# Kernel tuning notes

Measured on AMD Instinct MI355X. Metric: run time of the kernel, lower is better.

Reference implementation:

```python
import jax, jax.numpy as jnp
import numpy as np

T, B = 21, 4096
H, E, V = 1024, 50, 96
PAD = 0


def setup_inputs() -> dict:
    key = jax.random.key(0)
    ks = jax.random.split(key, 10)
    s_e = 1.0 / np.sqrt(H)  # torch LSTM init scale
    emb = jax.random.normal(ks[0], (V, E), jnp.float32)
    emb = emb.at[PAD].set(0.0)  # padding_idx row is zero
    return {
        "input_ids": jax.random.randint(ks[1], (T, B), 0, V),
        "h0": jax.random.normal(ks[2], (1, B, H), jnp.float32),
        "c0": jax.random.normal(ks[3], (1, B, H), jnp.float32),
        "emb": emb,
        "W_ih": jax.random.uniform(ks[4], (4 * H, E), jnp.float32, -s_e, s_e),
        "W_hh": jax.random.uniform(ks[5], (4 * H, H), jnp.float32, -s_e, s_e),
        "b_ih": jax.random.uniform(ks[6], (4 * H,), jnp.float32, -s_e, s_e),
        "b_hh": jax.random.uniform(ks[7], (4 * H,), jnp.float32, -s_e, s_e),
        "W_out": jax.random.uniform(ks[8], (V, H), jnp.float32, -s_e, s_e),
        "b_out": jax.random.uniform(ks[9], (V,), jnp.float32, -s_e, s_e),
    }


def reference(input_ids, h0, c0, emb, W_ih, W_hh, b_ih, b_hh, W_out, b_out):
    # char_embeds: (T, B, E)
    x = emb[input_ids]
    # Precompute input projections for all timesteps in one GEMM: (T, B, 4H)
    x_proj = jnp.einsum("tbe,ge->tbg", x, W_ih) + b_ih + b_hh

    def step(carry, xp_t):
        h, c = carry  # (B, H) each
        gates = xp_t + h @ W_hh.T  # (B, 4H), torch gate order i,f,g,o
        i, f, g, o = jnp.split(gates, 4, axis=-1)
        i = jax.nn.sigmoid(i)
        f = jax.nn.sigmoid(f)
        g = jnp.tanh(g)
        o = jax.nn.sigmoid(o)
        c = f * c + i * g
        h = o * jnp.tanh(c)
        return (h, c), h

    (h_T, c_T), h_ts = jax.lax.scan(step, (h0[0], c0[0]), x_proj)
    # char_output_projection: (T, B, V)
    scores = jnp.einsum("tbh,vh->tbv", h_ts, W_out) + b_out
    return scores, (h_T[None], c_T[None])
```

## Files before the change

kernel.cpp:

```cpp
#include <hip/hip_runtime.h>
#include <hip/hip_bf16.h>


#define T_STEPS 21
#define BSZ 4096
#define HDIM 1024
#define VOCAB 96
#define EDIM 50

typedef __attribute__((ext_vector_type(8))) short short8;
typedef __attribute__((ext_vector_type(4))) short shortx4;
typedef __attribute__((ext_vector_type(4))) float f32x4;

#define GLL16(g, l)                                                        \
  __builtin_amdgcn_global_load_lds(                                        \
      (const __attribute__((address_space(1))) void*)(g),                  \
      (__attribute__((address_space(3))) void*)(l), 16, 0, 0)

#define ASM_BARRIER() asm volatile("s_barrier" ::: "memory")
#define ASM_VMCNT4() asm volatile("s_waitcnt vmcnt(4)" ::: "memory")
#define ASM_VMCNT0() asm volatile("s_waitcnt vmcnt(0)" ::: "memory")

__device__ __forceinline__ float sigmoidf_fast(float x) {
  return 1.0f / (1.0f + __expf(-x));
}
__device__ __forceinline__ float tanhf_fast(float x) {
  return 2.0f / (1.0f + __expf(-2.0f * x)) - 1.0f;
}
__device__ __forceinline__ float b2f(short s) {
  return __uint_as_float(((unsigned int)(unsigned short)s) << 16);
}

__global__ void prep_convert(const float* __restrict__ Whh_f,
                             const float* __restrict__ Wout_f,
                             const float* __restrict__ h0,
                             __hip_bfloat16* __restrict__ Whh,
                             __hip_bfloat16* __restrict__ Wout,
                             __hip_bfloat16* __restrict__ hb0) {
  int idx = blockIdx.x * 256 + threadIdx.x;
  if (idx < 4 * HDIM * HDIM) {
    Whh[idx] = __float2bfloat16(Whh_f[idx]);
    hb0[idx] = __float2bfloat16(h0[idx]);
  }
  if (idx < VOCAB * HDIM) Wout[idx] = __float2bfloat16(Wout_f[idx]);
}

__global__ void prep_ptable(const float* __restrict__ emb,
                            const float* __restrict__ Wih,
                            const float* __restrict__ bih,
                            const float* __restrict__ bhh,
                            __hip_bfloat16* __restrict__ Pb) {
  int idx = blockIdx.x * 256 + threadIdx.x;
  int v = idx >> 12, g = idx & 4095;
  int gate = g >> 10, j = g & 1023;
  const float* er = emb + v * EDIM;
  const float* wr = Wih + g * EDIM;
  float s = bih[g] + bhh[g];
#pragma unroll 10
  for (int e = 0; e < EDIM; ++e) s += er[e] * wr[e];
  Pb[(size_t)(j >> 6) * 24576 + v * 256 + (j & 63) * 4 + gate] =
      __float2bfloat16(s);
}


#define STAGE_A(h, kt, b)                                                   \
  do {                                                                      \
    GLL16(hprev + aSrc[0] + (size_t)(h) * 131072 + (size_t)(kt) * 64,       \
          smem + ((b) << 16) + ((h) << 14) + aDst[0]);                      \
    GLL16(hprev + aSrc[1] + (size_t)(h) * 131072 + (size_t)(kt) * 64,       \
          smem + ((b) << 16) + ((h) << 14) + aDst[1]);                      \
  } while (0)

#define STAGE_B(h, kt, b)                                                   \
  do {                                                                      \
    GLL16(Whh + bSrc[h][0] + (size_t)(kt) * 64,                             \
          smem + ((b) << 16) + bDst[h][0]);                                 \
    GLL16(Whh + bSrc[h][1] + (size_t)(kt) * 64,                             \
          smem + ((b) << 16) + bDst[h][1]);                                 \
  } while (0)

#define PHASE(mh, nh, STAGE_STMT, VM_STMT)                                  \
  {                                                                         \
    short8 af[8], bf[4];                                                    \
    _Pragma("unroll") for (int mi2 = 0; mi2 < 4; ++mi2) {                   \
      af[mi2] = *(const short8*)&cA[((mh) * 128 + wr * 64 + mi2 * 16 +      \
                                     u16) * 64 + sl0];                      \
      af[4 + mi2] = *(const short8*)&cA[((mh) * 128 + wr * 64 + mi2 * 16 +  \
                                         u16) * 64 + sl1];                  \
    }                                                                       \
    _Pragma("unroll") for (int ni2 = 0; ni2 < 2; ++ni2) {                   \
      bf[ni2] = *(const short8*)&cB[(wc * 64 + (nh) * 32 + ni2 * 16 +       \
                                     u16) * 64 + sl0];                      \
      bf[2 + ni2] = *(const short8*)&cB[(wc * 64 + (nh) * 32 + ni2 * 16 +   \
                                         u16) * 64 + sl1];                  \
    }                                                                       \
    STAGE_STMT;                                                             \
    ASM_BARRIER();                                                          \
    __builtin_amdgcn_s_setprio(1);                                          \
    _Pragma("unroll") for (int mi2 = 0; mi2 < 4; ++mi2)                     \
        _Pragma("unroll") for (int ni2 = 0; ni2 < 2; ++ni2) {               \
      acc[(mh) * 4 + mi2][(nh) * 2 + ni2] =                                 \
          __builtin_amdgcn_mfma_f32_16x16x32_bf16(                          \
              af[mi2], bf[ni2], acc[(mh) * 4 + mi2][(nh) * 2 + ni2],        \
              0, 0, 0);                                                     \
      acc[(mh) * 4 + mi2][(nh) * 2 + ni2] =                                 \
          __builtin_amdgcn_mfma_f32_16x16x32_bf16(                          \
              af[4 + mi2], bf[2 + ni2],                                     \
              acc[(mh) * 4 + mi2][(nh) * 2 + ni2], 0, 0, 0);                \
    }                                                                       \
    __builtin_amdgcn_s_setprio(0);                                          \
    VM_STMT;                                                                \
    ASM_BARRIER();                                                          \
  }

template <bool LAST>
__global__ __launch_bounds__(512, 2) void lstm_step_kernel(
    const int* __restrict__ ids,
    const __hip_bfloat16* __restrict__ hprev,
    const __hip_bfloat16* __restrict__ Whh,
    const __hip_bfloat16* __restrict__ Pb,
    const float* __restrict__ c_in,
    float* __restrict__ c_out,
    __hip_bfloat16* __restrict__ hnext,
    float* __restrict__ hf32)
{
  __shared__ __align__(16) char smem[131072];

  const int tid = threadIdx.x;
  const int wid = tid >> 6;
  const int lane = tid & 63;
  const int wr = wid >> 2;
  const int wc = wid & 3;
  const int u16 = lane & 15;
  const int k16q = lane >> 4;
  const int u7 = u16 & 7;
  const int sl0 = (k16q ^ u7) * 8;
  const int sl1 = ((4 + k16q) ^ u7) * 8;

  const int bid = blockIdx.x;
  const int mt = (bid & 7) * 2 + ((bid >> 3) & 1);
  const int jt = bid >> 4;
  const int m0 = mt * 256;

  const int lrow = lane >> 3;
  const int swcol = ((lane & 7) ^ lrow) * 8;

  size_t aSrc[2];
  size_t bSrc[2][2];
  int aDst[2];
  int bDst[2][2];
#pragma unroll
  for (int q = 0; q < 2; ++q) {
    const int g = wid * 2 + q;
    aSrc[q] = (size_t)(m0 + g * 8 + lrow) * HDIM + swcol;
    aDst[q] = g * 1024;
#pragma unroll
    for (int h = 0; h < 2; ++h) {
      const int R = (g >> 2) * 64 + h * 32 + (g & 3) * 8;
      const int n = R + lrow;
      const int gate = (n >> 4) & 3;
      const int uo = (n >> 6) * 16 + (n & 15);
      bSrc[h][q] = (size_t)(gate * HDIM + jt * 64 + uo) * HDIM + swcol;
      bDst[h][q] = 32768 + R * 128;
    }
  }

  STAGE_A(0, 0, 0);
  STAGE_B(0, 0, 0);
  STAGE_A(1, 0, 0);
  STAGE_B(1, 0, 0);
  STAGE_A(0, 1, 1);
  STAGE_B(0, 1, 1);

  ASM_VMCNT4();
  ASM_BARRIER();

  f32x4 acc[8][4] = {};

#pragma unroll 2
  for (int k = 0; k < 16; ++k) {
    const int b = k & 1;
    const int nb = b ^ 1;
    const __hip_bfloat16* cA = (const __hip_bfloat16*)(smem + (b << 16));
    const __hip_bfloat16* cB =
        (const __hip_bfloat16*)(smem + (b << 16) + 32768);

    PHASE(0, 0, { if (k < 15) STAGE_A(1, k + 1, nb); }, {});
    PHASE(0, 1, { if (k < 15) STAGE_B(1, k + 1, nb); }, {});
    PHASE(1, 0, { if (k < 14) STAGE_A(0, k + 2, b); }, {});
    PHASE(1, 1, { if (k < 14) STAGE_B(0, k + 2, b); }, {
      if (k < 14) {
        ASM_VMCNT4();
      } else if (k == 14) {
        ASM_VMCNT0();
      }
    });
  }

  const int jcol = jt * 64 + wc * 16 + u16;
  float cpre[8][4];
#pragma unroll
  for (int mi = 0; mi < 8; ++mi)
#pragma unroll
    for (int r = 0; r < 4; ++r)
      cpre[mi][r] = c_in[(size_t)(m0 + (mi >> 2) * 128 + wr * 64 +
                                  (mi & 3) * 16 + k16q * 4 + r) *
                             HDIM +
                         jcol];

  {
    const __hip_bfloat16* Pbj = Pb + (size_t)jt * 24576;
#pragma unroll
    for (int i = 0; i < 6; ++i)
      GLL16(Pbj + (wid * 6 + i) * 512 + lane * 8,
            smem + (wid * 6 + i) * 1024);
  }
  ASM_VMCNT0();
  ASM_BARRIER();

  const __hip_bfloat16* sPb = (const __hip_bfloat16*)smem;
  const int uo4 = (wc * 16 + u16) * 4;
  const int rb = m0 + wr * 64 + k16q * 4;
#pragma unroll
  for (int mi = 0; mi < 8; ++mi) {
#pragma unroll
    for (int r = 0; r < 4; ++r) {
      const int row = rb + (mi >> 2) * 128 + (mi & 3) * 16 + r;
      const int id = ids[row];
      const shortx4 pv = *(const shortx4*)&sPb[id * 256 + uo4];
      float iv = acc[mi][0][r] + b2f(pv[0]);
      float fv = acc[mi][1][r] + b2f(pv[1]);
      float gv = acc[mi][2][r] + b2f(pv[2]);
      float ov = acc[mi][3][r] + b2f(pv[3]);
      iv = sigmoidf_fast(iv);
      fv = sigmoidf_fast(fv);
      gv = tanhf_fast(gv);
      ov = sigmoidf_fast(ov);
      const size_t off = (size_t)row * HDIM + jcol;
      const float cc = fv * cpre[mi][r] + iv * gv;
      c_out[off] = cc;
      const float hh = ov * tanhf_fast(cc);
      hnext[off] = __float2bfloat16(hh);
      if (LAST) hf32[off] = hh;
    }
  }
}

__global__ __launch_bounds__(256, 2) void scores_kernel(
    const __hip_bfloat16* __restrict__ h,
    const __hip_bfloat16* __restrict__ Wout,
    const float* __restrict__ bout,
    float* __restrict__ out)
{
  __shared__ __align__(16) __hip_bfloat16 sA[128 * 128];
  __shared__ __align__(16) __hip_bfloat16 sB[96 * 128];

  const int tid = threadIdx.x;
  const int wave = tid >> 6, lane = tid & 63;
  const int u16 = lane & 15, k16q = lane >> 4;
  const long r0 = (long)blockIdx.x * 128;

  f32x4 acc[2][6] = {};

  const int srow4 = lane >> 4;
  const int sslot = lane & 15;

  for (int k0 = 0; k0 < HDIM; k0 += 128) {
#pragma unroll
    for (int i = 0; i < 8; ++i) {
      int row = wave * 32 + i * 4 + srow4;
      int gg = sslot ^ (row & 15);
      GLL16(h + (r0 + row) * HDIM + k0 + gg * 8,
            &sA[(wave * 32 + i * 4) * 128]);
    }
#pragma unroll
    for (int i = 0; i < 6; ++i) {
      int row = wave * 24 + i * 4 + srow4;
      int gg = sslot ^ (row & 15);
      GLL16(Wout + (size_t)row * HDIM + k0 + gg * 8,
            &sB[(wave * 24 + i * 4) * 128]);
    }
    __syncthreads();
#pragma unroll
    for (int kk = 0; kk < 128; kk += 32) {
      const int sl = (((kk >> 3) + k16q) ^ u16) * 8;
      short8 af[2], bf[6];
#pragma unroll
      for (int mi = 0; mi < 2; ++mi)
        af[mi] = *(const short8*)&sA[(wave * 32 + mi * 16 + u16) * 128 + sl];
#pragma unroll
      for (int ni = 0; ni < 6; ++ni)
        bf[ni] = *(const short8*)&sB[(ni * 16 + u16) * 128 + sl];
#pragma unroll
      for (int mi = 0; mi < 2; ++mi)
#pragma unroll
        for (int ni = 0; ni < 6; ++ni)
          acc[mi][ni] = __builtin_amdgcn_mfma_f32_16x16x32_bf16(
              af[mi], bf[ni], acc[mi][ni], 0, 0, 0);
    }
    __syncthreads();
  }

#pragma unroll
  for (int ni = 0; ni < 6; ++ni) {
    int v = ni * 16 + u16;
    float bv = bout[v];
#pragma unroll
    for (int mi = 0; mi < 2; ++mi)
#pragma unroll
      for (int r = 0; r < 4; ++r) {
        long grow = r0 + wave * 32 + mi * 16 + k16q * 4 + r;
        out[grow * VOCAB + v] = acc[mi][ni][r] + bv;
      }
  }
}

extern "C" void kernel_launch(void* const* d_in, const int* in_sizes, int n_in,
                              void* d_out, int out_size, void* d_ws,
                              size_t ws_size, hipStream_t stream) {
  const int* ids = (const int*)d_in[0];
  const float* h0 = (const float*)d_in[1];
  const float* c0 = (const float*)d_in[2];
  const float* emb = (const float*)d_in[3];
  const float* Wih = (const float*)d_in[4];
  const float* Whh_f = (const float*)d_in[5];
  const float* bih = (const float*)d_in[6];
  const float* bhh = (const float*)d_in[7];
  const float* Wout_f = (const float*)d_in[8];
  const float* bout = (const float*)d_in[9];

  float* out = (float*)d_out;
  float* scores = out;
  float* hT = out + (size_t)T_STEPS * BSZ * VOCAB;
  float* cT = hT + (size_t)BSZ * HDIM;

  const size_t BH = (size_t)BSZ * HDIM;
  char* w = (char*)d_ws;
  __hip_bfloat16* Pb = (__hip_bfloat16*)w;   w += (size_t)16 * 24576 * 2;
  __hip_bfloat16* Whh = (__hip_bfloat16*)w;  w += (size_t)4 * HDIM * HDIM * 2;
  __hip_bfloat16* Wout = (__hip_bfloat16*)w; w += (size_t)VOCAB * HDIM * 2;
  __hip_bfloat16* hts = (__hip_bfloat16*)w;
  size_t base = (size_t)16 * 24576 * 2 + (size_t)4 * HDIM * HDIM * 2 +
                (size_t)VOCAB * HDIM * 2;
  const bool full = ws_size >= base + (size_t)(T_STEPS + 1) * BH * 2;

  prep_convert<<<dim3((4 * HDIM * HDIM + 255) / 256), dim3(256), 0, stream>>>(
      Whh_f, Wout_f, h0, Whh, Wout, hts);
  prep_ptable<<<dim3((VOCAB * 4096) / 256), dim3(256), 0, stream>>>(
      emb, Wih, bih, bhh, Pb);

  for (int t = 0; t < T_STEPS; ++t) {
    __hip_bfloat16* hp = hts + (full ? (size_t)t * BH : (size_t)(t & 1) * BH);
    __hip_bfloat16* hn =
        hts + (full ? (size_t)(t + 1) * BH : (size_t)((t + 1) & 1) * BH);
    const float* cin = (t == 0) ? c0 : cT;
    if (t == T_STEPS - 1) {
      lstm_step_kernel<true><<<dim3(256), dim3(512), 0, stream>>>(
          ids + (size_t)t * BSZ, hp, Whh, Pb, cin, cT, hn, hT);
    } else {
      lstm_step_kernel<false><<<dim3(256), dim3(512), 0, stream>>>(
          ids + (size_t)t * BSZ, hp, Whh, Pb, cin, cT, hn, nullptr);
    }
    if (!full) {
      scores_kernel<<<dim3(BSZ / 128), dim3(256), 0, stream>>>(
          hn, Wout, bout, scores + (size_t)t * BSZ * VOCAB);
    }
  }
  if (full) {
    scores_kernel<<<dim3(T_STEPS * BSZ / 128), dim3(256), 0, stream>>>(
        hts + BH, Wout, bout, scores);
  }
}
```

Baseline: 1.162 ms.

## Fuse LSTM timesteps into one persistent kernel with per-row-tile grid barriers

Replaces the 21 per-timestep LSTM kernel launches with a single persistent kernel of 256 blocks that loops over time. Each block synchronises only with the 16 blocks sharing its batch row tile through an atomic counter barrier. This removes launch overhead and the full-device drain between steps. It relies on all 256 blocks being co-resident (2 per CU via launch bounds) to avoid deadlock, and on counters reset in the prep kernel.

Measured after the change: 1.991 ms. 1.71x slower.

```diff
diff --git a/kernel.cpp b/kernel.cpp
--- a/kernel.cpp
+++ b/kernel.cpp
@@ -36,8 +36,10 @@
                              const float* __restrict__ h0,
                              __hip_bfloat16* __restrict__ Whh,
                              __hip_bfloat16* __restrict__ Wout,
-                             __hip_bfloat16* __restrict__ hb0) {
+                             __hip_bfloat16* __restrict__ hb0,
+                             int* __restrict__ bars) {
   int idx = blockIdx.x * 256 + threadIdx.x;
+  if (blockIdx.x == 0 && threadIdx.x < 16) bars[threadIdx.x] = 0;
   if (idx < 4 * HDIM * HDIM) {
     Whh[idx] = __float2bfloat16(Whh_f[idx]);
     hb0[idx] = __float2bfloat16(h0[idx]);
@@ -62,7 +64,6 @@
       __float2bfloat16(s);
 }
 
-
 #define STAGE_A(h, kt, b)                                                   \
   do {                                                                      \
     GLL16(hprev + aSrc[0] + (size_t)(h) * 131072 + (size_t)(kt) * 64,       \
@@ -113,137 +114,163 @@
     ASM_BARRIER();                                                          \
   }
 
+#define LSTM_SETUP()                                                        \
+  const int tid = threadIdx.x;                                              \
+  const int wid = tid >> 6;                                                 \
+  const int lane = tid & 63;                                                \
+  const int wr = wid >> 2;                                                  \
+  const int wc = wid & 3;                                                   \
+  const int u16 = lane & 15;                                                \
+  const int k16q = lane >> 4;                                               \
+  const int u7 = u16 & 7;                                                   \
+  const int sl0 = (k16q ^ u7) * 8;                                          \
+  const int sl1 = ((4 + k16q) ^ u7) * 8;                                    \
+  const int bid = blockIdx.x;                                               \
+  const int mt = (bid & 7) * 2 + ((bid >> 3) & 1);                          \
+  const int jt = bid >> 4;                                                  \
+  const int m0 = mt * 256;                                                  \
+  const int lrow = lane >> 3;                                               \
+  const int swcol = ((lane & 7) ^ lrow) * 8;                                \
+  size_t aSrc[2];                                                           \
+  size_t bSrc[2][2];                                                        \
+  int aDst[2];                                                              \
+  int bDst[2][2];                                                           \
+  _Pragma("unroll") for (int q = 0; q < 2; ++q) {                           \
+    const int g = wid * 2 + q;                                              \
+    aSrc[q] = (size_t)(m0 + g * 8 + lrow) * HDIM + swcol;                   \
+    aDst[q] = g * 1024;                                                     \
+    _Pragma("unroll") for (int h = 0; h < 2; ++h) {                         \
+      const int R = (g >> 2) * 64 + h * 32 + (g & 3) * 8;                   \
+      const int n = R + lrow;                                               \
+      const int gate = (n >> 4) & 3;                                        \
+      const int uo = (n >> 6) * 16 + (n & 15);                              \
+      bSrc[h][q] = (size_t)(gate * HDIM + jt * 64 + uo) * HDIM + swcol;     \
+      bDst[h][q] = 32768 + R * 128;                                         \
+    }                                                                       \
+  }
+
+#define LSTM_STEP_BODY(IS_LAST)                                             \
+  {                                                                         \
+    STAGE_A(0, 0, 0);                                                       \
+    STAGE_B(0, 0, 0);                                                       \
+    STAGE_A(1, 0, 0);                                                       \
+    STAGE_B(1, 0, 0);                                                       \
+    STAGE_A(0, 1, 1);                                                       \
+    STAGE_B(0, 1, 1);                                                       \
+    ASM_VMCNT4();                                                           \
+    ASM_BARRIER();                                                          \
+    f32x4 acc[8][4] = {};                                                   \
+    _Pragma("unroll 2") for (int k = 0; k < 16; ++k) {                      \
+      const int b = k & 1;                                                  \
+      const int nb = b ^ 1;                                                 \
+      const __hip_bfloat16* cA = (const __hip_bfloat16*)(smem + (b << 16)); \
+      const __hip_bfloat16* cB =                                            \
+          (const __hip_bfloat16*)(smem + (b << 16) + 32768);                \
+      PHASE(0, 0, { if (k < 15) STAGE_A(1, k + 1, nb); }, {});              \
+      PHASE(0, 1, { if (k < 15) STAGE_B(1, k + 1, nb); }, {});              \
+      PHASE(1, 0, { if (k < 14) STAGE_A(0, k + 2, b); }, {});               \
+      PHASE(1, 1, { if (k < 14) STAGE_B(0, k + 2, b); }, {                  \
+        if (k < 14) { ASM_VMCNT4(); } else if (k == 14) { ASM_VMCNT0(); }   \
+      });                                                                   \
+    }                                                                       \
+    const int jcol = jt * 64 + wc * 16 + u16;                               \
+    float cpre[8][4];                                                       \
+    _Pragma("unroll") for (int mi = 0; mi < 8; ++mi)                        \
+        _Pragma("unroll") for (int r = 0; r < 4; ++r)                       \
+            cpre[mi][r] = c_in_p[(size_t)(m0 + (mi >> 2) * 128 + wr * 64 +  \
+                                          (mi & 3) * 16 + k16q * 4 + r) *   \
+                                     HDIM +                                 \
+                                 jcol];                                     \
+    {                                                                       \
+      const __hip_bfloat16* Pbj = Pb + (size_t)jt * 24576;                  \
+      _Pragma("unroll") for (int i = 0; i < 6; ++i)                         \
+          GLL16(Pbj + (wid * 6 + i) * 512 + lane * 8,                       \
+                smem + (wid * 6 + i) * 1024);                               \
+    }                                                                       \
+    ASM_VMCNT0();                                                           \
+    ASM_BARRIER();                                                          \
+    const __hip_bfloat16* sPb = (const __hip_bfloat16*)smem;                \
+    const int uo4 = (wc * 16 + u16) * 4;                                    \
+    const int rb = m0 + wr * 64 + k16q * 4;                                 \
+    _Pragma("unroll") for (int mi = 0; mi < 8; ++mi) {                      \
+      _Pragma("unroll") for (int r = 0; r < 4; ++r) {                       \
+        const int row = rb + (mi >> 2) * 128 + (mi & 3) * 16 + r;           \
+        const int id = ids_t[row];                                          \
+        const shortx4 pv = *(const shortx4*)&sPb[id * 256 + uo4];           \
+        float iv = acc[mi][0][r] + b2f(pv[0]);                              \
+        float fv = acc[mi][1][r] + b2f(pv[1]);                              \
+        float gv = acc[mi][2][r] + b2f(pv[2]);                              \
+        float ov = acc[mi][3][r] + b2f(pv[3]);                              \
+        iv = sigmoidf_fast(iv);                                             \
+        fv = sigmoidf_fast(fv);                                             \
+        gv = tanhf_fast(gv);                                                \
+        ov = sigmoidf_fast(ov);                                             \
+        const size_t off = (size_t)row * HDIM + jcol;                       \
+        const float cc = fv * cpre[mi][r] + iv * gv;                        \
+        c_out_p[off] = cc;                                                  \
+        const float hh = ov * tanhf_fast(cc);                               \
+        hnext[off] = __float2bfloat16(hh);                                  \
+        if (IS_LAST) hf32_p[off] = hh;                                      \
+      }                                                                     \
+    }                                                                       \
+  }
+
+__global__ __launch_bounds__(512, 2) void lstm_persistent(
+    const int* __restrict__ ids,
+    const __hip_bfloat16* __restrict__ Whh,
+    const __hip_bfloat16* __restrict__ Pb,
+    const float* __restrict__ c0,
+    float* __restrict__ cT,
+    __hip_bfloat16* __restrict__ hts,
+    float* __restrict__ hT,
+    int* __restrict__ bars)
+{
+  __shared__ __align__(16) char smem[131072];
+  LSTM_SETUP();
+  const size_t BH = (size_t)BSZ * HDIM;
+
+#pragma unroll 1
+  for (int t = 0; t < T_STEPS; ++t) {
+    const __hip_bfloat16* hprev = hts + (size_t)t * BH;
+    __hip_bfloat16* hnext = hts + (size_t)(t + 1) * BH;
+    const float* c_in_p = (t == 0) ? c0 : cT;
+    float* c_out_p = cT;
+    const int* ids_t = ids + (size_t)t * BSZ;
+    float* hf32_p = hT;
+    const bool last = (t == T_STEPS - 1);
+
+    LSTM_STEP_BODY(last);
+
+    if (t < T_STEPS - 1) {
+      __syncthreads();
+      if (tid == 0) {
+        __hip_atomic_fetch_add(&bars[mt], 1, __ATOMIC_RELEASE,
+                               __HIP_MEMORY_SCOPE_AGENT);
+        const int target = 16 * (t + 1);
+        while (__hip_atomic_fetch_add(&bars[mt], 0, __ATOMIC_RELAXED,
+                                      __HIP_MEMORY_SCOPE_AGENT) < target)
+          __builtin_amdgcn_s_sleep(2);
+        (void)__hip_atomic_load(&bars[mt], __ATOMIC_ACQUIRE,
+                                __HIP_MEMORY_SCOPE_AGENT);
+      }
+      __syncthreads();
+    }
+  }
+}
+
 template <bool LAST>
 __global__ __launch_bounds__(512, 2) void lstm_step_kernel(
-    const int* __restrict__ ids,
+    const int* __restrict__ ids_t,
     const __hip_bfloat16* __restrict__ hprev,
     const __hip_bfloat16* __restrict__ Whh,
     const __hip_bfloat16* __restrict__ Pb,
-    const float* __restrict__ c_in,
-    float* __restrict__ c_out,
+    const float* __restrict__ c_in_p,
+    float* __restrict__ c_out_p,
     __hip_bfloat16* __restrict__ hnext,
-    float* __restrict__ hf32)
-{
+    float* __restrict__ hf32_p) {
   __shared__ __align__(16) char smem[131072];
-
-  const int tid = threadIdx.x;
-  const int wid = tid >> 6;
-  const int lane = tid & 63;
-  const int wr = wid >> 2;
-  const int wc = wid & 3;
-  const int u16 = lane & 15;
-  const int k16q = lane >> 4;
-  const int u7 = u16 & 7;
-  const int sl0 = (k16q ^ u7) * 8;
-  const int sl1 = ((4 + k16q) ^ u7) * 8;
-
-  const int bid = blockIdx.x;
-  const int mt = (bid & 7) * 2 + ((bid >> 3) & 1);
-  const int jt = bid >> 4;
-  const int m0 = mt * 256;
-
-  const int lrow = lane >> 3;
-  const int swcol = ((lane & 7) ^ lrow) * 8;
-
-  size_t aSrc[2];
-  size_t bSrc[2][2];
-  int aDst[2];
-  int bDst[2][2];
-#pragma unroll
-  for (int q = 0; q < 2; ++q) {
-    const int g = wid * 2 + q;
-    aSrc[q] = (size_t)(m0 + g * 8 + lrow) * HDIM + swcol;
-    aDst[q] = g * 1024;
-#pragma unroll
-    for (int h = 0; h < 2; ++h) {
-      const int R = (g >> 2) * 64 + h * 32 + (g & 3) * 8;
-      const int n = R + lrow;
-      const int gate = (n >> 4) & 3;
-      const int uo = (n >> 6) * 16 + (n & 15);
-      bSrc[h][q] = (size_t)(gate * HDIM + jt * 64 + uo) * HDIM + swcol;
-      bDst[h][q] = 32768 + R * 128;
-    }
-  }
-
-  STAGE_A(0, 0, 0);
-  STAGE_B(0, 0, 0);
-  STAGE_A(1, 0, 0);
-  STAGE_B(1, 0, 0);
-  STAGE_A(0, 1, 1);
-  STAGE_B(0, 1, 1);
-
-  ASM_VMCNT4();
-  ASM_BARRIER();
-
-  f32x4 acc[8][4] = {};
-
-#pragma unroll 2
-  for (int k = 0; k < 16; ++k) {
-    const int b = k & 1;
-    const int nb = b ^ 1;
-    const __hip_bfloat16* cA = (const __hip_bfloat16*)(smem + (b << 16));
-    const __hip_bfloat16* cB =
-        (const __hip_bfloat16*)(smem + (b << 16) + 32768);
-
-    PHASE(0, 0, { if (k < 15) STAGE_A(1, k + 1, nb); }, {});
-    PHASE(0, 1, { if (k < 15) STAGE_B(1, k + 1, nb); }, {});
-    PHASE(1, 0, { if (k < 14) STAGE_A(0, k + 2, b); }, {});
-    PHASE(1, 1, { if (k < 14) STAGE_B(0, k + 2, b); }, {
-      if (k < 14) {
-        ASM_VMCNT4();
-      } else if (k == 14) {
-        ASM_VMCNT0();
-      }
-    });
-  }
-
-  const int jcol = jt * 64 + wc * 16 + u16;
-  float cpre[8][4];
-#pragma unroll
-  for (int mi = 0; mi < 8; ++mi)
-#pragma unroll
-    for (int r = 0; r < 4; ++r)
-      cpre[mi][r] = c_in[(size_t)(m0 + (mi >> 2) * 128 + wr * 64 +
-                                  (mi & 3) * 16 + k16q * 4 + r) *
-                             HDIM +
-                         jcol];
-
-  {
-    const __hip_bfloat16* Pbj = Pb + (size_t)jt * 24576;
-#pragma unroll
-    for (int i = 0; i < 6; ++i)
-      GLL16(Pbj + (wid * 6 + i) * 512 + lane * 8,
-            smem + (wid * 6 + i) * 1024);
-  }
-  ASM_VMCNT0();
-  ASM_BARRIER();
-
-  const __hip_bfloat16* sPb = (const __hip_bfloat16*)smem;
-  const int uo4 = (wc * 16 + u16) * 4;
-  const int rb = m0 + wr * 64 + k16q * 4;
-#pragma unroll
-  for (int mi = 0; mi < 8; ++mi) {
-#pragma unroll
-    for (int r = 0; r < 4; ++r) {
-      const int row = rb + (mi >> 2) * 128 + (mi & 3) * 16 + r;
-      const int id = ids[row];
-      const shortx4 pv = *(const shortx4*)&sPb[id * 256 + uo4];
-      float iv = acc[mi][0][r] + b2f(pv[0]);
-      float fv = acc[mi][1][r] + b2f(pv[1]);
-      float gv = acc[mi][2][r] + b2f(pv[2]);
-      float ov = acc[mi][3][r] + b2f(pv[3]);
-      iv = sigmoidf_fast(iv);
-      fv = sigmoidf_fast(fv);
-      gv = tanhf_fast(gv);
-      ov = sigmoidf_fast(ov);
-      const size_t off = (size_t)row * HDIM + jcol;
-      const float cc = fv * cpre[mi][r] + iv * gv;
-      c_out[off] = cc;
-      const float hh = ov * tanhf_fast(cc);
-      hnext[off] = __float2bfloat16(hh);
-      if (LAST) hf32[off] = hh;
-    }
-  }
+  LSTM_SETUP();
+  LSTM_STEP_BODY(LAST);
 }
 
 __global__ __launch_bounds__(256, 2) void scores_kernel(
@@ -336,38 +363,39 @@
 
   const size_t BH = (size_t)BSZ * HDIM;
   char* w = (char*)d_ws;
+  int* bars = (int*)w;                       w += 256;
   __hip_bfloat16* Pb = (__hip_bfloat16*)w;   w += (size_t)16 * 24576 * 2;
   __hip_bfloat16* Whh = (__hip_bfloat16*)w;  w += (size_t)4 * HDIM * HDIM * 2;
   __hip_bfloat16* Wout = (__hip_bfloat16*)w; w += (size_t)VOCAB * HDIM * 2;
   __hip_bfloat16* hts = (__hip_bfloat16*)w;
-  size_t base = (size_t)16 * 24576 * 2 + (size_t)4 * HDIM * HDIM * 2 +
+  size_t base = 256 + (size_t)16 * 24576 * 2 + (size_t)4 * HDIM * HDIM * 2 +
                 (size_t)VOCAB * HDIM * 2;
   const bool full = ws_size >= base + (size_t)(T_STEPS + 1) * BH * 2;
 
   prep_convert<<<dim3((4 * HDIM * HDIM + 255) / 256), dim3(256), 0, stream>>>(
-      Whh_f, Wout_f, h0, Whh, Wout, hts);
+      Whh_f, Wout_f, h0, Whh, Wout, hts, bars);
   prep_ptable<<<dim3((VOCAB * 4096) / 256), dim3(256), 0, stream>>>(
       emb, Wih, bih, bhh, Pb);
 
-  for (int t = 0; t < T_STEPS; ++t) {
-    __hip_bfloat16* hp = hts + (full ? (size_t)t * BH : (size_t)(t & 1) * BH);
-    __hip_bfloat16* hn =
-        hts + (full ? (size_t)(t + 1) * BH : (size_t)((t + 1) & 1) * BH);
-    const float* cin = (t == 0) ? c0 : cT;
-    if (t == T_STEPS - 1) {
-      lstm_step_kernel<true><<<dim3(256), dim3(512), 0, stream>>>(
-          ids + (size_t)t * BSZ, hp, Whh, Pb, cin, cT, hn, hT);
-    } else {
-      lstm_step_kernel<false><<<dim3(256), dim3(512), 0, stream>>>(
-          ids + (size_t)t * BSZ, hp, Whh, Pb, cin, cT, hn, nullptr);
-    }
-    if (!full) {
+  if (full) {
+    lstm_persistent<<<dim3(256), dim3(512), 0, stream>>>(
+        ids, Whh, Pb, c0, cT, hts, hT, bars);
+    scores_kernel<<<dim3(T_STEPS * BSZ / 128), dim3(256), 0, stream>>>(
+        hts + BH, Wout, bout, scores);
+  } else {
+    for (int t = 0; t < T_STEPS; ++t) {
+      __hip_bfloat16* hp = hts + (size_t)(t & 1) * BH;
+      __hip_bfloat16* hn = hts + (size_t)((t + 1) & 1) * BH;
+      const float* cin = (t == 0) ? c0 : cT;
+      if (t == T_STEPS - 1) {
+        lstm_step_kernel<true><<<dim3(256), dim3(512), 0, stream>>>(
+            ids + (size_t)t * BSZ, hp, Whh, Pb, cin, cT, hn, hT);
+      } else {
+        lstm_step_kernel<false><<<dim3(256), dim3(512), 0, stream>>>(
+            ids + (size_t)t * BSZ, hp, Whh, Pb, cin, cT, hn, nullptr);
+      }
       scores_kernel<<<dim3(BSZ / 128), dim3(256), 0, stream>>>(
           hn, Wout, bout, scores + (size_t)t * BSZ * VOCAB);
     }
   }
-  if (full) {
-    scores_kernel<<<dim3(T_STEPS * BSZ / 128), dim3(256), 0, stream>>>(
-        hts + BH, Wout, bout, scores);
-  }
-}
+}
```
